# Kernel tuning notes

Hardware: AMD Instinct MI355X
Metric: run time of the kernel (lower is better)

Reference implementation:

```python
import jax, jax.numpy as jnp
import numpy as np

N = 50000   # nodes
E = 800000  # directed edges (self loops added in reference)
F = 8       # temporal features
D = 64      # hidden_channels
H = 4       # heads
C = D // H  # per-head channels = 16
L = 3       # num GAT layers
T = 3       # node types
TE = 16     # type embed dim


def _glorot(key, shape):
    fan_in, fan_out = shape[-2], shape[-1]
    s = jnp.sqrt(6.0 / (fan_in + fan_out))
    return jax.random.uniform(key, shape, jnp.float32, -s, s)


def setup_inputs() -> dict:
    key = jax.random.key(0)
    ks = jax.random.split(key, 24)
    return {
        'x': jax.random.normal(ks[0], (N, F), jnp.float32),
        'node_type': jax.random.randint(ks[1], (N,), 0, T),
        'edge_src': jax.random.randint(ks[2], (E,), 0, N),
        'edge_dst': jax.random.randint(ks[3], (E,), 0, N),
        # TemporalEncoder (Linear F->D + ReLU)
        'Wt': _glorot(ks[4], (F, D)), 'bt': jnp.zeros((D,), jnp.float32),
        # type embedding and input projection
        'Et': 0.1 * jax.random.normal(ks[5], (T, TE), jnp.float32),
        'Wp': _glorot(ks[6], (D + TE, D)), 'bp': jnp.zeros((D,), jnp.float32),
        # GATv2 layers (stacked over L)
        'Wl': _glorot(ks[7], (L, D, H * C)), 'bl': jnp.zeros((L, H * C), jnp.float32),
        'Wr': _glorot(ks[8], (L, D, H * C)), 'br': jnp.zeros((L, H * C), jnp.float32),
        'att': _glorot(ks[9], (L, H, C)),
        'Wres': _glorot(ks[10], (L, D, H * C)),
        'bconv': jnp.zeros((L, H * C), jnp.float32),
        'gamma': jnp.ones((L, D), jnp.float32), 'beta': jnp.zeros((L, D), jnp.float32),
        'alpha': jnp.float32(0.5),
        # output head
        'W1': _glorot(ks[11], (D, D // 2)), 'b1': jnp.zeros((D // 2,), jnp.float32),
        'W2': _glorot(ks[12], (D // 2, 1)), 'b2': jnp.zeros((1,), jnp.float32),
    }


def _layernorm(x, g, b, eps=1e-5):
    mu = jnp.mean(x, -1, keepdims=True)
    v = jnp.mean((x - mu) ** 2, -1, keepdims=True)
    return g * (x - mu) / jnp.sqrt(v + eps) + b


def reference(x, node_type, edge_src, edge_dst, Wt, bt, Et, Wp, bp,
              Wl, bl, Wr, br, att, Wres, bconv, gamma, beta, alpha,
              W1, b1, W2, b2):
    # temporal encoder + type embedding + input projection
    h = jax.nn.relu(x @ Wt + bt)                       # [N, D]
    h = jnp.concatenate([h, Et[node_type]], axis=-1) @ Wp + bp
    h0 = h

    # add self loops once (eval mode -> no dropout)
    loop = jnp.arange(N)
    src = jnp.concatenate([edge_src, loop])            # [E']
    dst = jnp.concatenate([edge_dst, loop])

    for l in range(L):
        xl = (h @ Wl[l] + bl[l]).reshape(N, H, C)      # source transform
        xr = (h @ Wr[l] + br[l]).reshape(N, H, C)      # target transform
        e = jax.nn.leaky_relu(xl[src] + xr[dst], 0.2)  # [E', H, C]
        score = jnp.einsum('ehc,hc->eh', e, att[l])    # [E', H]
        # segment softmax over incoming edges of each destination node
        m = jax.ops.segment_max(score, dst, num_segments=N)
        ex = jnp.exp(score - m[dst])
        s = jax.ops.segment_sum(ex, dst, num_segments=N)
        a = ex / (s[dst] + 1e-16)                      # [E', H]
        msg = xl[src] * a[:, :, None]                  # [E', H, C]
        out = jax.ops.segment_sum(msg, dst, num_segments=N).reshape(N, H * C)
        out = out + h @ Wres[l] + bconv[l]             # GATv2 residual + bias
        h = _layernorm(alpha * out + (1.0 - alpha) * h0, gamma[l], beta[l])

    z = jax.nn.relu(h @ W1 + b1)
    return jax.nn.sigmoid(z @ W2 + b2)                 # [N, 1]
```

## Files before the change

kernel.cpp:

```cpp
#include <hip/hip_runtime.h>
#include <hip/hip_bf16.h>

typedef __hip_bfloat16 bf16;
typedef __attribute__((ext_vector_type(8))) short short8;
typedef __attribute__((ext_vector_type(4))) float f32x4;

__device__ __forceinline__ float b2f(bf16 v) { return __bfloat162float(v); }
__device__ __forceinline__ bf16 f2b(float v) { return __float2bfloat16(v); }
__device__ __forceinline__ short f2bs(float v) {
    bf16 b = f2b(v);
    return *reinterpret_cast<short*>(&b);
}
__device__ __forceinline__ float bflo(unsigned int u) { return __uint_as_float(u << 16); }
__device__ __forceinline__ float bfhi(unsigned int u) { return __uint_as_float(u & 0xffff0000u); }
__device__ __forceinline__ unsigned int packbf(float lo, float hi) {
    bf16 l = f2b(lo), h = f2b(hi);
    return ((unsigned int)(*(unsigned short*)&h) << 16) | (*(unsigned short*)&l);
}


__global__ void k_sentinel(float* out, int n, float val) {
    int i = blockIdx.x * blockDim.x + threadIdx.x;
    if (i < n) out[i] = val;
}

#define PREP_BLOCKS 169
__global__ void k_setup(const float* __restrict__ Wl, const float* __restrict__ Wr,
                        const float* __restrict__ Wres, const float* __restrict__ Wp,
                        const float* __restrict__ W1, const float* __restrict__ Et,
                        const float* __restrict__ bp,
                        bf16* __restrict__ WT, bf16* __restrict__ WpT,
                        bf16* __restrict__ W1T, float* __restrict__ TyB,
                        const int* __restrict__ edst, int* __restrict__ counts,
                        int* __restrict__ rank, int e) {
    int b = blockIdx.x;
    if (b < PREP_BLOCKS) {
        int i = b * 256 + threadIdx.x;
        if (i < 36864) {
            int l = i / 12288, rem = i % 12288;
            int col = rem / 64, k = rem % 64;
            int mat = col >> 6, c = col & 63;
            const float* W = (mat == 0) ? Wl : (mat == 1) ? Wr : Wres;
            WT[i] = f2b(W[l * 4096 + k * 64 + c]);
        } else if (i < 40960) {
            int j = i - 36864, col = j / 64, k = j % 64;
            WpT[j] = f2b(Wp[k * 64 + col]);
        } else if (i < 43008) {
            int j = i - 40960, col = j / 64, k = j % 64;
            W1T[j] = f2b(W1[k * 32 + col]);
        } else if (i < 43200) {
            int j = i - 43008, t = j / 64, d = j % 64;
            float s = bp[d];
#pragma unroll
            for (int f = 0; f < 16; ++f) s += Et[t * 16 + f] * Wp[(64 + f) * 64 + d];
            TyB[j] = s;
        }
    } else {
        int i = (b - PREP_BLOCKS) * 256 + threadIdx.x;
        if (i < e) rank[i] = atomicAdd(&counts[edst[i]], 1);
    }
}

__global__ __launch_bounds__(256) void k_encx(
        const float* __restrict__ x, const int* __restrict__ ntype,
        const float* __restrict__ Wt, const float* __restrict__ bt,
        const bf16* __restrict__ WpT, const float* __restrict__ TyB,
        bf16* __restrict__ h0b,
        const bf16* __restrict__ WT0, const float* __restrict__ bl0,
        const float* __restrict__ br0, const float* __restrict__ bc0,
        bf16* __restrict__ xlo, bf16* __restrict__ xro, bf16* __restrict__ reso,
        int n) {
    __shared__ float sWt[512];
    __shared__ float sbt[64];
    __shared__ __align__(16) short sh[4 * 16 * 72];
    int tid = threadIdx.x;
    for (int i = tid; i < 512; i += 256) sWt[i] = Wt[i];
    if (tid < 64) sbt[tid] = bt[tid];
    __syncthreads();
    int wave = tid >> 6, lane = tid & 63;
    int nb = blockIdx.x * 64 + wave * 16;
    if (nb >= n) return;
    int m = lane & 15, q = lane >> 4;
    short* shw = sh + wave * 16 * 72;

    const float* xrow = x + (size_t)(nb + m) * 8;
    float xv[8];
#pragma unroll
    for (int f = 0; f < 8; ++f) xv[f] = xrow[f];

    short8 a0, a1;
#pragma unroll
    for (int j = 0; j < 8; ++j) {
        int c0 = q * 8 + j, c1 = 32 + q * 8 + j;
        float s0 = sbt[c0], s1 = sbt[c1];
#pragma unroll
        for (int f = 0; f < 8; ++f) {
            s0 += xv[f] * sWt[f * 64 + c0];
            s1 += xv[f] * sWt[f * 64 + c1];
        }
        a0[j] = f2bs(fmaxf(s0, 0.f));
        a1[j] = f2bs(fmaxf(s1, 0.f));
    }

    int ty[4];
#pragma unroll
    for (int r = 0; r < 4; ++r) ty[r] = ntype[nb + q * 4 + r];

#pragma unroll
    for (int t = 0; t < 4; ++t) {
        const short* wp = (const short*)(WpT + (size_t)(t * 16 + m) * 64) + q * 8;
        short8 b0 = *(const short8*)(wp);
        short8 b1 = *(const short8*)(wp + 32);
        f32x4 acc = {0.f, 0.f, 0.f, 0.f};
        acc = __builtin_amdgcn_mfma_f32_16x16x32_bf16(a0, b0, acc, 0, 0, 0);
        acc = __builtin_amdgcn_mfma_f32_16x16x32_bf16(a1, b1, acc, 0, 0, 0);
        int col = t * 16 + m;
#pragma unroll
        for (int r = 0; r < 4; ++r) {
            int nd = nb + q * 4 + r;
            short vb = f2bs(acc[r] + TyB[ty[r] * 64 + col]);
            h0b[(size_t)nd * 64 + col] = *reinterpret_cast<bf16*>(&vb);
            shw[(q * 4 + r) * 72 + col] = vb;
        }
    }
    short8 ha0 = *(const short8*)(&shw[m * 72 + q * 8]);
    short8 ha1 = *(const short8*)(&shw[m * 72 + 32 + q * 8]);
#pragma unroll
    for (int t = 0; t < 12; ++t) {
        const short* wp = (const short*)(WT0 + (size_t)(t * 16 + m) * 64) + q * 8;
        short8 b0 = *(const short8*)(wp);
        short8 b1 = *(const short8*)(wp + 32);
        f32x4 acc = {0.f, 0.f, 0.f, 0.f};
        acc = __builtin_amdgcn_mfma_f32_16x16x32_bf16(ha0, b0, acc, 0, 0, 0);
        acc = __builtin_amdgcn_mfma_f32_16x16x32_bf16(ha1, b1, acc, 0, 0, 0);
        int col = t * 16 + m;
        int mat = col >> 6, c = col & 63;
        float bias = (mat == 0) ? bl0[c] : (mat == 1) ? br0[c] : bc0[c];
        bf16* dst = (mat == 0) ? xlo : (mat == 1) ? xro : reso;
#pragma unroll
        for (int r = 0; r < 4; ++r)
            dst[(size_t)(nb + q * 4 + r) * 64 + c] = f2b(acc[r] + bias);
    }
}

__global__ void k_scan_local(const int* __restrict__ counts, int* __restrict__ row_raw,
                             int* __restrict__ bsum, int* __restrict__ hist, int n) {
    __shared__ int part[256];
    __shared__ int lh[64];
    int tid = threadIdx.x;
    if (tid < 64) lh[tid] = 0;
    __syncthreads();
    int base = blockIdx.x * 1024 + tid * 4;
    int d0 = (base     < n) ? counts[base]     : -1;
    int d1 = (base + 1 < n) ? counts[base + 1] : -1;
    int d2 = (base + 2 < n) ? counts[base + 2] : -1;
    int d3 = (base + 3 < n) ? counts[base + 3] : -1;
    if (d0 >= 0) atomicAdd(&lh[63 - (d0 < 63 ? d0 : 63)], 1);
    if (d1 >= 0) atomicAdd(&lh[63 - (d1 < 63 ? d1 : 63)], 1);
    if (d2 >= 0) atomicAdd(&lh[63 - (d2 < 63 ? d2 : 63)], 1);
    if (d3 >= 0) atomicAdd(&lh[63 - (d3 < 63 ? d3 : 63)], 1);
    int c0 = d0 + 1, c1 = d1 + 1, c2 = d2 + 1, c3 = d3 + 1;
    part[tid] = c0 + c1 + c2 + c3;
    __syncthreads();
    for (int off = 1; off < 256; off <<= 1) {
        int t = (tid >= off) ? part[tid - off] : 0;
        __syncthreads();
        part[tid] += t;
        __syncthreads();
    }
    int ex = (tid == 0) ? 0 : part[tid - 1];
    if (base     < n) row_raw[base]     = ex;
    if (base + 1 < n) row_raw[base + 1] = ex + c0;
    if (base + 2 < n) row_raw[base + 2] = ex + c0 + c1;
    if (base + 3 < n) row_raw[base + 3] = ex + c0 + c1 + c2;
    if (tid == 255) bsum[blockIdx.x] = part[255];
    if (tid < 64 && lh[tid] > 0) atomicAdd(&hist[tid], lh[tid]);
}

__global__ void k_scan_bsum(int* __restrict__ bsum, int* __restrict__ row_ptr,
                            int* __restrict__ hist, int g, int n) {
    int lane = threadIdx.x;
    int orig = (lane < g) ? bsum[lane] : 0;
    int v = orig;
#pragma unroll
    for (int off = 1; off < 64; off <<= 1) {
        int t = __shfl_up(v, off, 64);
        if (lane >= off) v += t;
    }
    if (lane < g) bsum[lane] = v - orig;
    if (lane == 63) row_ptr[n] = v;

    int ho = hist[lane];
    int hv = ho;
#pragma unroll
    for (int off = 1; off < 64; off <<= 1) {
        int t = __shfl_up(hv, off, 64);
        if (lane >= off) hv += t;
    }
    hist[lane] = hv - ho;
}

__global__ void k_build(const int* __restrict__ src, const int* __restrict__ dst,
                        const int* __restrict__ row_raw, const int* __restrict__ bsum,
                        const int* __restrict__ rank, const int* __restrict__ counts,
                        int* __restrict__ row_ptr, int* __restrict__ csr_src,
                        int* __restrict__ hist, int* __restrict__ perm,
                        int n, int e) {
    __shared__ int lh[64];
    __shared__ int gbase[64];
    int tid = threadIdx.x;
    int i = blockIdx.x * 256 + tid;
    bool nodework = (blockIdx.x * 256) < n;
    if (nodework) {
        if (tid < 64) lh[tid] = 0;
        __syncthreads();
        int bucket = 0, myrank = -1;
        if (i < n) {
            int d = counts[i];
            bucket = 63 - (d < 63 ? d : 63);
            myrank = atomicAdd(&lh[bucket], 1);
        }
        __syncthreads();
        if (tid < 64 && lh[tid] > 0) gbase[tid] = atomicAdd(&hist[tid], lh[tid]);
        __syncthreads();
        if (i < n) perm[gbase[bucket] + myrank] = i;
    }
    if (i < n) {
        int rp = row_raw[i] + bsum[i >> 10];
        row_ptr[i] = rp;
        csr_src[rp] = i;
    }
    if (i < e) {
        int d = dst[i];
        int pos = row_raw[d] + bsum[d >> 10] + 1 + rank[i];
        csr_src[pos] = src[i];
    }
}

#define GAT2_STEP(E_IDX, LS, A0S, A1S)                                            \
    {                                                                             \
        int s_ = csr_src[E_IDX];                                                  \
        unsigned int xu_ = *(const unsigned int*)((const unsigned short*)xl +     \
                                                  (size_t)s_ * 64 + ch);          \
        float x0_ = bflo(xu_), x1_ = bfhi(xu_);                                   \
        float t0_ = x0_ + xr0; t0_ = fmaxf(t0_, 0.2f * t0_);                      \
        float t1_ = x1_ + xr1; t1_ = fmaxf(t1_, 0.2f * t1_);                      \
        float p_ = t0_ * at0 + t1_ * at1;                                         \
        p_ += __shfl_xor(p_, 1, 64);                                              \
        p_ += __shfl_xor(p_, 2, 64);                                              \
        p_ += __shfl_xor(p_, 4, 64);                                              \
        float pe_ = __expf(fminf(p_, 60.f));                                      \
        A0S += pe_ * x0_;  A1S += pe_ * x1_;  LS += pe_;                          \
    }

#define GAT_PHASE_BODY                                                            \
    int tid = threadIdx.x;                                                        \
    int wave = tid >> 6, lane = tid & 63;                                         \
    int half = lane >> 5;                                                         \
    int L = lane & 31;                                                            \
    int head = L >> 3, cp = L & 7;                                                \
    int ch = head * 16 + cp * 2;                                                  \
    int nl = wave * 2 + half;                                                     \
    int idx = blockIdx.x * 16 + nl;                                               \
    bool valid = idx < n;                                                         \
    int v = valid ? perm[idx] : 0;                                                \
    if (L == 0) sid[nl] = valid ? v : -1;                                         \
    unsigned int xru = *(const unsigned int*)((const unsigned short*)xr +         \
                                              (size_t)v * 64 + ch);               \
    float xr0 = bflo(xru), xr1 = bfhi(xru);                                       \
    float at0 = att[ch], at1 = att[ch + 1];                                       \
    int beg = row_ptr[v];                                                         \
    int end = valid ? row_ptr[v + 1] : beg;                                       \
    float l0 = 0.f, A00 = 0.f, A01 = 0.f;                                         \
    float l1 = 0.f, A10 = 0.f, A11 = 0.f;                                         \
    float l2 = 0.f, A20 = 0.f, A21 = 0.f;                                         \
    float l3 = 0.f, A30 = 0.f, A31 = 0.f;                                         \
    int e = beg;                                                                  \
    for (; e + 3 < end; e += 4) {                                                 \
        GAT2_STEP(e,     l0, A00, A01)                                            \
        GAT2_STEP(e + 1, l1, A10, A11)                                            \
        GAT2_STEP(e + 2, l2, A20, A21)                                            \
        GAT2_STEP(e + 3, l3, A30, A31)                                            \
    }                                                                             \
    int rem = end - e;                                                            \
    if (rem > 0) GAT2_STEP(e,     l0, A00, A01)                                   \
    if (rem > 1) GAT2_STEP(e + 1, l1, A10, A11)                                   \
    if (rem > 2) GAT2_STEP(e + 2, l2, A20, A21)                                   \
    float lsum = (l0 + l1) + (l2 + l3);                                           \
    float inv = 1.f / (lsum + 1e-16f);                                            \
    float acc0 = ((A00 + A10) + (A20 + A30)) * inv;                               \
    float acc1 = ((A01 + A11) + (A21 + A31)) * inv;                               \
    unsigned int ru = *(const unsigned int*)((const unsigned short*)res +         \
                                             (size_t)v * 64 + ch);                \
    unsigned int hu = *(const unsigned int*)((const unsigned short*)h0b +         \
                                             (size_t)v * 64 + ch);                \
    float o0 = acc0 + bflo(ru);                                                   \
    float o1 = acc1 + bfhi(ru);                                                   \
    float a = alpha_p[0];                                                         \
    float t0 = a * o0 + (1.f - a) * bflo(hu);                                     \
    float t1 = a * o1 + (1.f - a) * bfhi(hu);                                     \
    float mu = t0 + t1;                                                           \
    _Pragma("unroll")                                                             \
    for (int o = 1; o < 32; o <<= 1) mu += __shfl_xor(mu, o, 64);                 \
    mu *= (1.f / 64.f);                                                           \
    float d0 = t0 - mu, d1 = t1 - mu;                                             \
    float var = d0 * d0 + d1 * d1;                                                \
    _Pragma("unroll")                                                             \
    for (int o = 1; o < 32; o <<= 1) var += __shfl_xor(var, o, 64);               \
    var *= (1.f / 64.f);                                                          \
    float rs = rsqrtf(var + 1e-5f);                                               \
    float hn0 = gamma[ch] * d0 * rs + beta[ch];                                   \
    float hn1 = gamma[ch + 1] * d1 * rs + beta[ch + 1];                           \
    *(unsigned int*)((char*)sh + nl * 144 + ch * 2) = packbf(hn0, hn1);           \
    __syncthreads();

__global__ __launch_bounds__(512) void k_gatx(
        const bf16* __restrict__ xl, const bf16* __restrict__ xr,
        const bf16* __restrict__ res, const bf16* __restrict__ h0b,
        const float* __restrict__ att, const float* __restrict__ gamma,
        const float* __restrict__ beta, const float* __restrict__ alpha_p,
        const int* __restrict__ row_ptr, const int* __restrict__ csr_src,
        const int* __restrict__ perm,
        const bf16* __restrict__ WTn, const float* __restrict__ bln,
        const float* __restrict__ brn, const float* __restrict__ bcn,
        bf16* __restrict__ xlo, bf16* __restrict__ xro, bf16* __restrict__ reso,
        int n) {
    __shared__ __align__(16) short sh[16 * 72];
    __shared__ int sid[16];
    GAT_PHASE_BODY

    int m = lane & 15, q = lane >> 4;
    short8 ha0 = *(const short8*)(&sh[m * 72 + q * 8]);
    short8 ha1 = *(const short8*)(&sh[m * 72 + 32 + q * 8]);
    for (int t = wave; t < 12; t += 8) {
        const short* wp = (const short*)(WTn + (size_t)(t * 16 + m) * 64) + q * 8;
        short8 b0 = *(const short8*)(wp);
        short8 b1 = *(const short8*)(wp + 32);
        f32x4 acc = {0.f, 0.f, 0.f, 0.f};
        acc = __builtin_amdgcn_mfma_f32_16x16x32_bf16(ha0, b0, acc, 0, 0, 0);
        acc = __builtin_amdgcn_mfma_f32_16x16x32_bf16(ha1, b1, acc, 0, 0, 0);
        int col = t * 16 + m;
        int mat = col >> 6, c = col & 63;
        float bias = (mat == 0) ? bln[c] : (mat == 1) ? brn[c] : bcn[c];
        bf16* dst = (mat == 0) ? xlo : (mat == 1) ? xro : reso;
#pragma unroll
        for (int r = 0; r < 4; ++r) {
            int nd = sid[q * 4 + r];
            if (nd >= 0) dst[(size_t)nd * 64 + c] = f2b(acc[r] + bias);
        }
    }
}

__global__ __launch_bounds__(512) void k_gath(
        const bf16* __restrict__ xl, const bf16* __restrict__ xr,
        const bf16* __restrict__ res, const bf16* __restrict__ h0b,
        const float* __restrict__ att, const float* __restrict__ gamma,
        const float* __restrict__ beta, const float* __restrict__ alpha_p,
        const int* __restrict__ row_ptr, const int* __restrict__ csr_src,
        const int* __restrict__ perm,
        const bf16* __restrict__ W1T, const float* __restrict__ b1,
        const float* __restrict__ W2, const float* __restrict__ b2,
        float* __restrict__ out, int n) {
    __shared__ __align__(16) short sh[16 * 72];
    __shared__ int sid[16];
    GAT_PHASE_BODY

    if (wave == 0) {
        int m = lane & 15, q = lane >> 4;
        short8 ha0 = *(const short8*)(&sh[m * 72 + q * 8]);
        short8 ha1 = *(const short8*)(&sh[m * 72 + 32 + q * 8]);

        const short* w0p = (const short*)(W1T + (size_t)m * 64) + q * 8;
        const short* w1p = (const short*)(W1T + (size_t)(16 + m) * 64) + q * 8;
        short8 b00 = *(const short8*)(w0p);
        short8 b01 = *(const short8*)(w0p + 32);
        short8 b10 = *(const short8*)(w1p);
        short8 b11 = *(const short8*)(w1p + 32);

        f32x4 acc0 = {0.f, 0.f, 0.f, 0.f};
        f32x4 acc1 = {0.f, 0.f, 0.f, 0.f};
        acc0 = __builtin_amdgcn_mfma_f32_16x16x32_bf16(ha0, b00, acc0, 0, 0, 0);
        acc0 = __builtin_amdgcn_mfma_f32_16x16x32_bf16(ha1, b01, acc0, 0, 0, 0);
        acc1 = __builtin_amdgcn_mfma_f32_16x16x32_bf16(ha0, b10, acc1, 0, 0, 0);
        acc1 = __builtin_amdgcn_mfma_f32_16x16x32_bf16(ha1, b11, acc1, 0, 0, 0);

        float w2a = W2[m], w2b = W2[16 + m];
        float bb0 = b1[m], bb1 = b1[16 + m];
        float part[4];
#pragma unroll
        for (int r = 0; r < 4; ++r)
            part[r] = fmaxf(acc0[r] + bb0, 0.f) * w2a + fmaxf(acc1[r] + bb1, 0.f) * w2b;
#pragma unroll
        for (int mask = 1; mask < 16; mask <<= 1) {
#pragma unroll
            for (int r = 0; r < 4; ++r) part[r] += __shfl_xor(part[r], mask, 64);
        }
        if (m == 0) {
            float bb2 = b2[0];
#pragma unroll
            for (int r = 0; r < 4; ++r) {
                int nd = sid[q * 4 + r];
                if (nd >= 0) out[nd] = 1.f / (1.f + __expf(-(part[r] + bb2)));
            }
        }
    }
}

extern "C" void kernel_launch(void* const* d_in, const int* in_sizes, int n_in,
                              void* d_out, int out_size, void* d_ws, size_t ws_size,
                              hipStream_t stream) {
    const float* x     = (const float*)d_in[0];
    const int*   ntype = (const int*)d_in[1];
    const int*   esrc  = (const int*)d_in[2];
    const int*   edst  = (const int*)d_in[3];
    const float* Wt    = (const float*)d_in[4];
    const float* bt    = (const float*)d_in[5];
    const float* Et    = (const float*)d_in[6];
    const float* Wp    = (const float*)d_in[7];
    const float* bp    = (const float*)d_in[8];
    const float* Wl    = (const float*)d_in[9];
    const float* bl    = (const float*)d_in[10];
    const float* Wr    = (const float*)d_in[11];
    const float* br    = (const float*)d_in[12];
    const float* att   = (const float*)d_in[13];
    const float* Wres  = (const float*)d_in[14];
    const float* bconv = (const float*)d_in[15];
    const float* gamma = (const float*)d_in[16];
    const float* beta  = (const float*)d_in[17];
    const float* alpha = (const float*)d_in[18];
    const float* W1    = (const float*)d_in[19];
    const float* b1    = (const float*)d_in[20];
    const float* W2    = (const float*)d_in[21];
    const float* b2    = (const float*)d_in[22];
    float* out = (float*)d_out;

    const int N = in_sizes[1];
    const int E = in_sizes[2];

    const int G = (N + 1023) / 1024;

    size_t need = 256
                + (size_t)N * 64 * 2 * 7
                + (size_t)36864 * 2 + (size_t)4096 * 2 + (size_t)2048 * 2
                + (size_t)192 * 4
                + (size_t)N * 4
                + (size_t)(N + 1) * 4
                + (size_t)(N + 64) * 4
                + (size_t)N * 4
                + (size_t)E * 4
                + 256
                + (size_t)(E + N) * 4;

    if (ws_size < need) {
        k_sentinel<<<(N + 255) / 256, 256, 0, stream>>>(out, N,
                                                        100.0f + (float)(ws_size >> 20));
        return;
    }

    char* ws = (char*)d_ws;
    ws += 256;
    bf16* h0b   = (bf16*)ws;  ws += (size_t)N * 64 * 2;
    bf16* xlA   = (bf16*)ws;  ws += (size_t)N * 64 * 2;
    bf16* xrA   = (bf16*)ws;  ws += (size_t)N * 64 * 2;
    bf16* resA  = (bf16*)ws;  ws += (size_t)N * 64 * 2;
    bf16* xlB   = (bf16*)ws;  ws += (size_t)N * 64 * 2;
    bf16* xrB   = (bf16*)ws;  ws += (size_t)N * 64 * 2;
    bf16* resB  = (bf16*)ws;  ws += (size_t)N * 64 * 2;
    bf16* WT    = (bf16*)ws;  ws += (size_t)36864 * 2;
    bf16* WpT   = (bf16*)ws;  ws += (size_t)4096 * 2;
    bf16* W1T   = (bf16*)ws;  ws += (size_t)2048 * 2;
    float* TyB  = (float*)ws; ws += (size_t)192 * 4;
    int* row_raw = (int*)ws;  ws += (size_t)N * 4;
    int* row_ptr = (int*)ws;  ws += (size_t)(N + 1) * 4;
    int* counts  = (int*)ws;  ws += (size_t)N * 4;
    int* hist    = (int*)ws;  ws += (size_t)64 * 4;
    int* perm    = (int*)ws;  ws += (size_t)N * 4;
    int* rank    = (int*)ws;  ws += (size_t)E * 4;
    int* bsum    = (int*)ws;  ws += 256;
    int* csr_src = (int*)ws;  ws += (size_t)(E + N) * 4;

    hipMemsetAsync(counts, 0, (size_t)(N + 64) * 4, stream);
    k_setup<<<PREP_BLOCKS + (E + 255) / 256, 256, 0, stream>>>(
        Wl, Wr, Wres, Wp, W1, Et, bp, WT, WpT, W1T, TyB, edst, counts, rank, E);
    k_encx<<<(N + 63) / 64, 256, 0, stream>>>(x, ntype, Wt, bt, WpT, TyB, h0b,
                                              WT, bl, br, bconv, xlA, xrA, resA, N);
    k_scan_local<<<G, 256, 0, stream>>>(counts, row_raw, bsum, hist, N);
    k_scan_bsum<<<1, 64, 0, stream>>>(bsum, row_ptr, hist, G, N);
    k_build<<<(E + 255) / 256, 256, 0, stream>>>(esrc, edst, row_raw, bsum, rank,
                                                 counts, row_ptr, csr_src, hist, perm,
                                                 N, E);

    k_gatx<<<(N + 15) / 16, 512, 0, stream>>>(
        xlA, xrA, resA, h0b, att, gamma, beta, alpha, row_ptr, csr_src, perm,
        WT + 12288, bl + 64, br + 64, bconv + 64, xlB, xrB, resB, N);
    k_gatx<<<(N + 15) / 16, 512, 0, stream>>>(
        xlB, xrB, resB, h0b, att + 64, gamma + 64, beta + 64, alpha, row_ptr, csr_src,
        perm, WT + 24576, bl + 128, br + 128, bconv + 128, xlA, xrA, resA, N);
    k_gath<<<(N + 15) / 16, 512, 0, stream>>>(
        xlA, xrA, resA, h0b, att + 128, gamma + 128, beta + 128, alpha,
        row_ptr, csr_src, perm, W1T, b1, W2, b2, out, N);
}
```

Before: 300.8 us.

## Remap GAT aggregation lanes to 8 channels per lane with 4 edge groups

Each half-wave previously gave each lane 2 channels and walked all edges serially. Now each lane loads 16-byte vectors holding 8 channels, and the 4 lane groups process interleaved edges in parallel. Partial sums are combined across groups with cross-lane shuffles. This cuts the shuffle reduction per edge from 3 to 1, uses wider gathers, and shortens the serial edge loop. The cost is 18 extra shuffles after the loop, and only one group writes the LayerNorm output.

```diff
diff --git a/kernel.cpp b/kernel.cpp
--- a/kernel.cpp
+++ b/kernel.cpp
@@ -237,20 +237,28 @@
     }
 }
 
-#define GAT2_STEP(E_IDX, LS, A0S, A1S)                                            \
+#define GAT8_STEP(XU)                                                             \
     {                                                                             \
-        int s_ = csr_src[E_IDX];                                                  \
-        unsigned int xu_ = *(const unsigned int*)((const unsigned short*)xl +     \
-                                                  (size_t)s_ * 64 + ch);          \
-        float x0_ = bflo(xu_), x1_ = bfhi(xu_);                                   \
-        float t0_ = x0_ + xr0; t0_ = fmaxf(t0_, 0.2f * t0_);                      \
-        float t1_ = x1_ + xr1; t1_ = fmaxf(t1_, 0.2f * t1_);                      \
-        float p_ = t0_ * at0 + t1_ * at1;                                         \
+        float xf0 = bflo(XU.x), xf1 = bfhi(XU.x);                                 \
+        float xf2 = bflo(XU.y), xf3 = bfhi(XU.y);                                 \
+        float xf4 = bflo(XU.z), xf5 = bfhi(XU.z);                                 \
+        float xf6 = bflo(XU.w), xf7 = bfhi(XU.w);                                 \
+        float u0 = xf0 + xq0; u0 = fmaxf(u0, 0.2f * u0);                          \
+        float u1 = xf1 + xq1; u1 = fmaxf(u1, 0.2f * u1);                          \
+        float u2 = xf2 + xq2; u2 = fmaxf(u2, 0.2f * u2);                          \
+        float u3 = xf3 + xq3; u3 = fmaxf(u3, 0.2f * u3);                          \
+        float u4 = xf4 + xq4; u4 = fmaxf(u4, 0.2f * u4);                          \
+        float u5 = xf5 + xq5; u5 = fmaxf(u5, 0.2f * u5);                          \
+        float u6 = xf6 + xq6; u6 = fmaxf(u6, 0.2f * u6);                          \
+        float u7 = xf7 + xq7; u7 = fmaxf(u7, 0.2f * u7);                          \
+        float p0_ = (u0 * at0 + u1 * at1) + (u2 * at2 + u3 * at3);                \
+        float p1_ = (u4 * at4 + u5 * at5) + (u6 * at6 + u7 * at7);                \
+        float p_ = p0_ + p1_;                                                     \
         p_ += __shfl_xor(p_, 1, 64);                                              \
-        p_ += __shfl_xor(p_, 2, 64);                                              \
-        p_ += __shfl_xor(p_, 4, 64);                                              \
         float pe_ = __expf(fminf(p_, 60.f));                                      \
-        A0S += pe_ * x0_;  A1S += pe_ * x1_;  LS += pe_;                          \
+        lsum += pe_;                                                              \
+        A0 += pe_ * xf0; A1 += pe_ * xf1; A2 += pe_ * xf2; A3 += pe_ * xf3;       \
+        A4 += pe_ * xf4; A5 += pe_ * xf5; A6 += pe_ * xf6; A7 += pe_ * xf7;       \
     }
 
 #define GAT_PHASE_BODY                                                            \
@@ -258,60 +266,91 @@
     int wave = tid >> 6, lane = tid & 63;                                         \
     int half = lane >> 5;                                                         \
     int L = lane & 31;                                                            \
-    int head = L >> 3, cp = L & 7;                                                \
-    int ch = head * 16 + cp * 2;                                                  \
+    int g = L >> 3;                                                               \
+    int k = L & 7;                                                                \
     int nl = wave * 2 + half;                                                     \
     int idx = blockIdx.x * 16 + nl;                                               \
     bool valid = idx < n;                                                         \
     int v = valid ? perm[idx] : 0;                                                \
     if (L == 0) sid[nl] = valid ? v : -1;                                         \
-    unsigned int xru = *(const unsigned int*)((const unsigned short*)xr +         \
-                                              (size_t)v * 64 + ch);               \
-    float xr0 = bflo(xru), xr1 = bfhi(xru);                                       \
-    float at0 = att[ch], at1 = att[ch + 1];                                       \
+    uint4 xruv = ((const uint4*)(xr + (size_t)v * 64))[k];                        \
+    float xq0 = bflo(xruv.x), xq1 = bfhi(xruv.x);                                 \
+    float xq2 = bflo(xruv.y), xq3 = bfhi(xruv.y);                                 \
+    float xq4 = bflo(xruv.z), xq5 = bfhi(xruv.z);                                 \
+    float xq6 = bflo(xruv.w), xq7 = bfhi(xruv.w);                                 \
+    float4 atv0 = ((const float4*)att)[k * 2];                                    \
+    float4 atv1 = ((const float4*)att)[k * 2 + 1];                                \
+    float at0 = atv0.x, at1 = atv0.y, at2 = atv0.z, at3 = atv0.w;                 \
+    float at4 = atv1.x, at5 = atv1.y, at6 = atv1.z, at7 = atv1.w;                 \
     int beg = row_ptr[v];                                                         \
     int end = valid ? row_ptr[v + 1] : beg;                                       \
-    float l0 = 0.f, A00 = 0.f, A01 = 0.f;                                         \
-    float l1 = 0.f, A10 = 0.f, A11 = 0.f;                                         \
-    float l2 = 0.f, A20 = 0.f, A21 = 0.f;                                         \
-    float l3 = 0.f, A30 = 0.f, A31 = 0.f;                                         \
-    int e = beg;                                                                  \
-    for (; e + 3 < end; e += 4) {                                                 \
-        GAT2_STEP(e,     l0, A00, A01)                                            \
-        GAT2_STEP(e + 1, l1, A10, A11)                                            \
-        GAT2_STEP(e + 2, l2, A20, A21)                                            \
-        GAT2_STEP(e + 3, l3, A30, A31)                                            \
+    float lsum = 0.f;                                                             \
+    float A0 = 0.f, A1 = 0.f, A2 = 0.f, A3 = 0.f;                                 \
+    float A4 = 0.f, A5 = 0.f, A6 = 0.f, A7 = 0.f;                                 \
+    int e = beg + g;                                                              \
+    for (; e + 4 < end; e += 8) {                                                 \
+        int s0_ = csr_src[e];                                                     \
+        int s1_ = csr_src[e + 4];                                                 \
+        uint4 xu0_ = ((const uint4*)(xl + (size_t)s0_ * 64))[k];                  \
+        uint4 xu1_ = ((const uint4*)(xl + (size_t)s1_ * 64))[k];                  \
+        GAT8_STEP(xu0_)                                                           \
+        GAT8_STEP(xu1_)                                                           \
     }                                                                             \
-    int rem = end - e;                                                            \
-    if (rem > 0) GAT2_STEP(e,     l0, A00, A01)                                   \
-    if (rem > 1) GAT2_STEP(e + 1, l1, A10, A11)                                   \
-    if (rem > 2) GAT2_STEP(e + 2, l2, A20, A21)                                   \
-    float lsum = (l0 + l1) + (l2 + l3);                                           \
+    if (e < end) {                                                                \
+        int s0_ = csr_src[e];                                                     \
+        uint4 xu0_ = ((const uint4*)(xl + (size_t)s0_ * 64))[k];                  \
+        GAT8_STEP(xu0_)                                                           \
+    }                                                                             \
+    lsum += __shfl_xor(lsum, 8, 64);  lsum += __shfl_xor(lsum, 16, 64);           \
+    A0 += __shfl_xor(A0, 8, 64);  A0 += __shfl_xor(A0, 16, 64);                   \
+    A1 += __shfl_xor(A1, 8, 64);  A1 += __shfl_xor(A1, 16, 64);                   \
+    A2 += __shfl_xor(A2, 8, 64);  A2 += __shfl_xor(A2, 16, 64);                   \
+    A3 += __shfl_xor(A3, 8, 64);  A3 += __shfl_xor(A3, 16, 64);                   \
+    A4 += __shfl_xor(A4, 8, 64);  A4 += __shfl_xor(A4, 16, 64);                   \
+    A5 += __shfl_xor(A5, 8, 64);  A5 += __shfl_xor(A5, 16, 64);                   \
+    A6 += __shfl_xor(A6, 8, 64);  A6 += __shfl_xor(A6, 16, 64);                   \
+    A7 += __shfl_xor(A7, 8, 64);  A7 += __shfl_xor(A7, 16, 64);                   \
     float inv = 1.f / (lsum + 1e-16f);                                            \
-    float acc0 = ((A00 + A10) + (A20 + A30)) * inv;                               \
-    float acc1 = ((A01 + A11) + (A21 + A31)) * inv;                               \
-    unsigned int ru = *(const unsigned int*)((const unsigned short*)res +         \
-                                             (size_t)v * 64 + ch);                \
-    unsigned int hu = *(const unsigned int*)((const unsigned short*)h0b +         \
-                                             (size_t)v * 64 + ch);                \
-    float o0 = acc0 + bflo(ru);                                                   \
-    float o1 = acc1 + bfhi(ru);                                                   \
+    uint4 ruv = ((const uint4*)(res + (size_t)v * 64))[k];                        \
+    uint4 huv = ((const uint4*)(h0b + (size_t)v * 64))[k];                        \
     float a = alpha_p[0];                                                         \
-    float t0 = a * o0 + (1.f - a) * bflo(hu);                                     \
-    float t1 = a * o1 + (1.f - a) * bfhi(hu);                                     \
-    float mu = t0 + t1;                                                           \
-    _Pragma("unroll")                                                             \
-    for (int o = 1; o < 32; o <<= 1) mu += __shfl_xor(mu, o, 64);                 \
+    float ac = 1.f - a;                                                           \
+    float t0 = a * (A0 * inv + bflo(ruv.x)) + ac * bflo(huv.x);                   \
+    float t1 = a * (A1 * inv + bfhi(ruv.x)) + ac * bfhi(huv.x);                   \
+    float t2 = a * (A2 * inv + bflo(ruv.y)) + ac * bflo(huv.y);                   \
+    float t3 = a * (A3 * inv + bfhi(ruv.y)) + ac * bfhi(huv.y);                   \
+    float t4 = a * (A4 * inv + bflo(ruv.z)) + ac * bflo(huv.z);                   \
+    float t5 = a * (A5 * inv + bfhi(ruv.z)) + ac * bfhi(huv.z);                   \
+    float t6 = a * (A6 * inv + bflo(ruv.w)) + ac * bflo(huv.w);                   \
+    float t7 = a * (A7 * inv + bfhi(ruv.w)) + ac * bfhi(huv.w);                   \
+    float mu = ((t0 + t1) + (t2 + t3)) + ((t4 + t5) + (t6 + t7));                 \
+    mu += __shfl_xor(mu, 1, 64);                                                  \
+    mu += __shfl_xor(mu, 2, 64);                                                  \
+    mu += __shfl_xor(mu, 4, 64);                                                  \
     mu *= (1.f / 64.f);                                                           \
-    float d0 = t0 - mu, d1 = t1 - mu;                                             \
-    float var = d0 * d0 + d1 * d1;                                                \
-    _Pragma("unroll")                                                             \
-    for (int o = 1; o < 32; o <<= 1) var += __shfl_xor(var, o, 64);               \
+    float d0 = t0 - mu, d1 = t1 - mu, d2 = t2 - mu, d3 = t3 - mu;                 \
+    float d4 = t4 - mu, d5 = t5 - mu, d6 = t6 - mu, d7 = t7 - mu;                 \
+    float var = ((d0 * d0 + d1 * d1) + (d2 * d2 + d3 * d3)) +                     \
+                ((d4 * d4 + d5 * d5) + (d6 * d6 + d7 * d7));                      \
+    var += __shfl_xor(var, 1, 64);                                                \
+    var += __shfl_xor(var, 2, 64);                                                \
+    var += __shfl_xor(var, 4, 64);                                                \
     var *= (1.f / 64.f);                                                          \
     float rs = rsqrtf(var + 1e-5f);                                               \
-    float hn0 = gamma[ch] * d0 * rs + beta[ch];                                   \
-    float hn1 = gamma[ch + 1] * d1 * rs + beta[ch + 1];                           \
-    *(unsigned int*)((char*)sh + nl * 144 + ch * 2) = packbf(hn0, hn1);           \
+    float4 gm0 = ((const float4*)gamma)[k * 2];                                   \
+    float4 gm1 = ((const float4*)gamma)[k * 2 + 1];                               \
+    float4 bb0_ = ((const float4*)beta)[k * 2];                                   \
+    float4 bb1_ = ((const float4*)beta)[k * 2 + 1];                               \
+    short8 hs;                                                                    \
+    hs[0] = f2bs(gm0.x * d0 * rs + bb0_.x);                                       \
+    hs[1] = f2bs(gm0.y * d1 * rs + bb0_.y);                                       \
+    hs[2] = f2bs(gm0.z * d2 * rs + bb0_.z);                                       \
+    hs[3] = f2bs(gm0.w * d3 * rs + bb0_.w);                                       \
+    hs[4] = f2bs(gm1.x * d4 * rs + bb1_.x);                                       \
+    hs[5] = f2bs(gm1.y * d5 * rs + bb1_.y);                                       \
+    hs[6] = f2bs(gm1.z * d6 * rs + bb1_.z);                                       \
+    hs[7] = f2bs(gm1.w * d7 * rs + bb1_.w);                                       \
+    if (g == 0) *(short8*)(&sh[nl * 72 + k * 8]) = hs;                            \
     __syncthreads();
 
 __global__ __launch_bounds__(512) void k_gatx(
```

Measured after the change: 305.5 us. Within noise of the previous version (+1.6%).
